# Performance work log

Measured on AMD Instinct MI355X. Metric: run time of the kernel, lower is better.

Reference implementation:

```python
import jax, jax.numpy as jnp
import numpy as np

D_IN = 1024
D_OUT = 1024
NUM_HEADS = 16
HEAD_DIM = D_OUT // NUM_HEADS


def setup_inputs() -> dict:
    key = jax.random.key(0)
    ks = jax.random.split(key, 6)
    B, S = 2, 2048
    scale = 1.0 / np.sqrt(D_IN)
    x = jax.random.normal(ks[0], (B, S, D_IN), dtype=jnp.float32)
    # Linear weights stored torch-style as [out_features, in_features]
    Wq = jax.random.normal(ks[1], (D_OUT, D_IN), dtype=jnp.float32) * scale
    Wk = jax.random.normal(ks[2], (D_OUT, D_IN), dtype=jnp.float32) * scale
    Wv = jax.random.normal(ks[3], (D_OUT, D_IN), dtype=jnp.float32) * scale
    Wo = jax.random.normal(ks[4], (D_OUT, D_IN), dtype=jnp.float32) * scale
    bo = jax.random.normal(ks[5], (D_OUT,), dtype=jnp.float32) * 0.01
    return {"x": x, "Wq": Wq, "Wk": Wk, "Wv": Wv, "Wo": Wo, "bo": bo}


def reference(x, Wq, Wk, Wv, Wo, bo):
    B, S, _ = x.shape
    H, hd = NUM_HEADS, HEAD_DIM
    # QKV projections (qkv_bias=False), split into heads: [B, H, S, hd]
    q = (x @ Wq.T).reshape(B, S, H, hd).transpose(0, 2, 1, 3)
    k = (x @ Wk.T).reshape(B, S, H, hd).transpose(0, 2, 1, 3)
    v = (x @ Wv.T).reshape(B, S, H, hd).transpose(0, 2, 1, 3)
    # scaled causal attention scores [B, H, S, S]
    scores = jnp.einsum("bhqd,bhkd->bhqk", q, k) / jnp.sqrt(jnp.float32(hd))
    causal = jnp.tril(jnp.ones((S, S), dtype=bool))
    scores = jnp.where(causal, scores, jnp.finfo(scores.dtype).min)
    attn = jax.nn.softmax(scores, axis=-1)  # dropout p=0.0 -> identity
    ctx = jnp.einsum("bhqk,bhkd->bhqd", attn, v)  # [B, H, S, hd]
    ctx = ctx.transpose(0, 2, 1, 3).reshape(B, S, H * hd)
    return ctx @ Wo.T + bo
```

## Files before the change

kernel.cpp:

```cpp
#include <hip/hip_runtime.h>
#include <hip/hip_bf16.h>

#define AS1 __attribute__((address_space(1)))
#define AS3 __attribute__((address_space(3)))

typedef __attribute__((ext_vector_type(4))) float floatx4;
typedef __attribute__((ext_vector_type(8))) short bf16x8;
typedef unsigned short u16;
typedef unsigned int u32;

__device__ __forceinline__ u16 f2b(float f) {
  u32 u = __builtin_bit_cast(u32, f);
  u += 0x7fffu + ((u >> 16) & 1u);
  return (u16)(u >> 16);
}
__device__ __forceinline__ u32 pk2(float lo, float hi) {
  __hip_bfloat162 h = __float22bfloat162_rn(float2{lo, hi});
  u32 u;
  __builtin_memcpy(&u, &h, 4);
  return u;
}
__device__ __forceinline__ bf16x8 cvt8(float4 a, float4 b) {
  uint4 u{pk2(a.x, a.y), pk2(a.z, a.w), pk2(b.x, b.y), pk2(b.z, b.w)};
  return __builtin_bit_cast(bf16x8, u);
}

__device__ __forceinline__ void gld16(const void* g, AS3 u32* l) {
  __builtin_amdgcn_global_load_lds((const AS1 u32*)(const AS1 void*)g, l, 16,
                                   0, 0);
}

#define QSCALE 0.18033688011112042f
#define QSHIFT 14.4269504088896f

__global__ __launch_bounds__(256) void cvt_all(
    const float* __restrict__ x, const float* __restrict__ wq,
    const float* __restrict__ wk, const float* __restrict__ wv,
    const float* __restrict__ wo, u16* __restrict__ xb, u16* __restrict__ wqb,
    u16* __restrict__ wkb, u16* __restrict__ wvb, u16* __restrict__ wob) {
  const int i = blockIdx.x * 256 + threadIdx.x;
  const float* src;
  u16* dst;
  int off;
  if (i < 524288) {
    src = x; dst = xb; off = i;
  } else {
    const int j = i - 524288;
    const int wsel = j >> 17;
    off = j & 131071;
    src = (wsel == 0) ? wq : (wsel == 1) ? wk : (wsel == 2) ? wv : wo;
    dst = (wsel == 0) ? wqb : (wsel == 1) ? wkb : (wsel == 2) ? wvb : wob;
  }
  const float4* p = (const float4*)(src + (size_t)off * 8);
  *(bf16x8*)(dst + (size_t)off * 8) = cvt8(p[0], p[1]);
}

__device__ __forceinline__ void gemm_bf16(const u16* __restrict__ A,
                                          const u16* __restrict__ B, short* sA,
                                          short* sB, floatx4 acc[4][4]) {
  const int tid = threadIdx.x;
  const int lane = tid & 63;
  const int w = tid >> 6;
  const int l15 = lane & 15, quad = lane >> 4;
  const int wm = w >> 1, wn = w & 1;

  const u16* ga = A + ((size_t)(w * 32 + (lane >> 2))) * 1024 + (lane & 3) * 8;
  const u16* gb = B + ((size_t)(w * 32 + (lane >> 2))) * 1024 + (lane & 3) * 8;
  AS3 u32* la = (AS3 u32*)(AS3 short*)sA + w * 512;
  AS3 u32* lb = (AS3 u32*)(AS3 short*)sB + w * 512;

  for (int kt = 0; kt < 32; ++kt) {
    __syncthreads();
    gld16(ga, la);
    gld16(ga + (size_t)16 * 1024, la + 256);
    gld16(gb, lb);
    gld16(gb + (size_t)16 * 1024, lb + 256);
    ga += 32;
    gb += 32;
    __syncthreads();

    bf16x8 af[4], bfr[4];
#pragma unroll
    for (int mc = 0; mc < 4; ++mc)
      af[mc] = *(const bf16x8*)&sA[(wm * 64 + mc * 16 + l15) * 32 + quad * 8];
#pragma unroll
    for (int nc = 0; nc < 4; ++nc)
      bfr[nc] = *(const bf16x8*)&sB[(wn * 64 + nc * 16 + l15) * 32 + quad * 8];
#pragma unroll
    for (int mc = 0; mc < 4; ++mc)
#pragma unroll
      for (int nc = 0; nc < 4; ++nc)
        acc[mc][nc] = __builtin_amdgcn_mfma_f32_16x16x32_bf16(
            af[mc], bfr[nc], acc[mc][nc], 0, 0, 0);
  }
}

__device__ __forceinline__ void qkv_epilogue(floatx4 acc[4][4], int m0, int nb,
                                             int sel, u16* __restrict__ Q,
                                             u16* __restrict__ K,
                                             u16* __restrict__ Vt) {
  const int tid = threadIdx.x;
  const int lane = tid & 63, w = tid >> 6;
  const int l15 = lane & 15, quad = lane >> 4;
  const int wm = w >> 1, wn = w & 1;
#pragma unroll
  for (int mc = 0; mc < 4; ++mc) {
#pragma unroll
    for (int nc = 0; nc < 4; ++nc) {
      const int nn = nb + wn * 64 + nc * 16 + l15;
      const int h = nn >> 6, d = nn & 63;
#pragma unroll
      for (int r = 0; r < 4; ++r) {
        const int m = m0 + wm * 64 + mc * 16 + quad * 4 + r;
        const int b = m >> 11, s = m & 2047;
        const int bh = b * 16 + h;
        float av = acc[mc][nc][r];
        if (sel == 0) av *= QSCALE;
        const u16 v = f2b(av);
        if (sel == 0)
          Q[((size_t)bh * 2048 + s) * 64 + d] = v;
        else if (sel == 1)
          K[((size_t)bh * 2048 + s) * 64 + d] = v;
        else
          Vt[((size_t)bh * 64 + d) * 2048 + s] = v;
      }
    }
  }
}

__global__ __launch_bounds__(256) void qkv_gemm_b(
    const u16* __restrict__ xb, const u16* __restrict__ Wqb,
    const u16* __restrict__ Wkb, const u16* __restrict__ Wvb,
    u16* __restrict__ Q, u16* __restrict__ K, u16* __restrict__ Vt) {
  __shared__ __align__(16) short smem[2 * 128 * 32];
  const int m0 = blockIdx.x * 128;
  const int by = blockIdx.y;
  const int sel = by >> 3;
  const int nb = (by & 7) * 128;
  const u16* W = (sel == 0) ? Wqb : (sel == 1) ? Wkb : Wvb;

  floatx4 acc[4][4];
#pragma unroll
  for (int i = 0; i < 4; i++)
#pragma unroll
    for (int j = 0; j < 4; j++) acc[i][j] = (floatx4)0.0f;
  gemm_bf16(xb + (size_t)m0 * 1024, W + (size_t)nb * 1024, smem,
            smem + 128 * 32, acc);
  qkv_epilogue(acc, m0, nb, sel, Q, K, Vt);
}

__global__ __launch_bounds__(256) void out_gemm_b(const u16* __restrict__ ctx,
                                                  const u16* __restrict__ Wob,
                                                  const float* __restrict__ bo,
                                                  float* __restrict__ out) {
  __shared__ __align__(16) short smem[128 * 32 + 64 * 32];
  const int tid = threadIdx.x;
  const int lane = tid & 63, w = tid >> 6;
  const int l15 = lane & 15, quad = lane >> 4;
  const int m0 = blockIdx.x * 128;
  const int n0 = blockIdx.y * 64;
  short* sA = smem;
  short* sB = smem + 128 * 32;

  const u16* ga = ctx + ((size_t)(m0 + w * 32 + (lane >> 2))) * 1024 +
                  (lane & 3) * 8;
  const u16* gb = Wob + ((size_t)(n0 + w * 16 + (lane >> 2))) * 1024 +
                  (lane & 3) * 8;
  AS3 u32* la = (AS3 u32*)(AS3 short*)sA + w * 512;
  AS3 u32* lb = (AS3 u32*)(AS3 short*)sB + w * 256;

  floatx4 acc[2][4];
#pragma unroll
  for (int i = 0; i < 2; i++)
#pragma unroll
    for (int j = 0; j < 4; j++) acc[i][j] = (floatx4)0.0f;

  for (int kt = 0; kt < 32; ++kt) {
    __syncthreads();
    gld16(ga, la);
    gld16(ga + (size_t)16 * 1024, la + 256);
    gld16(gb, lb);
    ga += 32;
    gb += 32;
    __syncthreads();

    bf16x8 af[2], bfr[4];
#pragma unroll
    for (int mc = 0; mc < 2; ++mc)
      af[mc] = *(const bf16x8*)&sA[(w * 32 + mc * 16 + l15) * 32 + quad * 8];
#pragma unroll
    for (int nc = 0; nc < 4; ++nc)
      bfr[nc] = *(const bf16x8*)&sB[(nc * 16 + l15) * 32 + quad * 8];
#pragma unroll
    for (int mc = 0; mc < 2; ++mc)
#pragma unroll
      for (int nc = 0; nc < 4; ++nc)
        acc[mc][nc] = __builtin_amdgcn_mfma_f32_16x16x32_bf16(
            af[mc], bfr[nc], acc[mc][nc], 0, 0, 0);
  }

#pragma unroll
  for (int mc = 0; mc < 2; ++mc)
#pragma unroll
    for (int nc = 0; nc < 4; ++nc) {
      const int n = n0 + nc * 16 + l15;
      const float bias = bo[n];
#pragma unroll
      for (int r = 0; r < 4; ++r) {
        const int m = m0 + w * 32 + mc * 16 + quad * 4 + r;
        out[(size_t)m * 1024 + n] = acc[mc][nc][r] + bias;
      }
    }
}

template <bool F32A>
__device__ __forceinline__ void gemm128(const void* __restrict__ A,
                                        const float* __restrict__ B, short* sA,
                                        short* sB, floatx4 acc[4][4]) {
  const int tid = threadIdx.x;
  const int lane = tid & 63;
  const int w = tid >> 6;
  const int l15 = lane & 15, quad = lane >> 4;
  const int wm = w >> 1, wn = w & 1;
  const int srow = tid >> 1;
  const int scb = (tid & 1) * 16;

  float4 pa[4], pb[4];
  int4 pa16[2];
  if constexpr (F32A) {
    const float* ap = (const float*)A + (size_t)srow * 1024 + scb;
    pa[0] = ((const float4*)ap)[0]; pa[1] = ((const float4*)ap)[1];
    pa[2] = ((const float4*)ap)[2]; pa[3] = ((const float4*)ap)[3];
  } else {
    const u16* ap = (const u16*)A + (size_t)srow * 1024 + scb;
    pa16[0] = ((const int4*)ap)[0]; pa16[1] = ((const int4*)ap)[1];
  }
  {
    const float* bp = B + (size_t)srow * 1024 + scb;
    pb[0] = ((const float4*)bp)[0]; pb[1] = ((const float4*)bp)[1];
    pb[2] = ((const float4*)bp)[2]; pb[3] = ((const float4*)bp)[3];
  }

  for (int kt = 0; kt < 32; ++kt) {
    __syncthreads();
    if constexpr (F32A) {
      *(bf16x8*)&sA[srow * 40 + scb] = cvt8(pa[0], pa[1]);
      *(bf16x8*)&sA[srow * 40 + scb + 8] = cvt8(pa[2], pa[3]);
    } else {
      *(int4*)&sA[srow * 40 + scb] = pa16[0];
      *(int4*)&sA[srow * 40 + scb + 8] = pa16[1];
    }
    *(bf16x8*)&sB[srow * 40 + scb] = cvt8(pb[0], pb[1]);
    *(bf16x8*)&sB[srow * 40 + scb + 8] = cvt8(pb[2], pb[3]);
    __syncthreads();

    if (kt < 31) {
      const int k0 = (kt + 1) * 32;
      if constexpr (F32A) {
        const float* ap = (const float*)A + (size_t)srow * 1024 + k0 + scb;
        pa[0] = ((const float4*)ap)[0]; pa[1] = ((const float4*)ap)[1];
        pa[2] = ((const float4*)ap)[2]; pa[3] = ((const float4*)ap)[3];
      } else {
        const u16* ap = (const u16*)A + (size_t)srow * 1024 + k0 + scb;
        pa16[0] = ((const int4*)ap)[0]; pa16[1] = ((const int4*)ap)[1];
      }
      const float* bp = B + (size_t)srow * 1024 + k0 + scb;
      pb[0] = ((const float4*)bp)[0]; pb[1] = ((const float4*)bp)[1];
      pb[2] = ((const float4*)bp)[2]; pb[3] = ((const float4*)bp)[3];
    }

    bf16x8 af[4], bfr[4];
#pragma unroll
    for (int mc = 0; mc < 4; ++mc)
      af[mc] = *(const bf16x8*)&sA[(wm * 64 + mc * 16 + l15) * 40 + quad * 8];
#pragma unroll
    for (int nc = 0; nc < 4; ++nc)
      bfr[nc] = *(const bf16x8*)&sB[(wn * 64 + nc * 16 + l15) * 40 + quad * 8];
#pragma unroll
    for (int mc = 0; mc < 4; ++mc)
#pragma unroll
      for (int nc = 0; nc < 4; ++nc)
        acc[mc][nc] = __builtin_amdgcn_mfma_f32_16x16x32_bf16(
            af[mc], bfr[nc], acc[mc][nc], 0, 0, 0);
  }
}

__global__ __launch_bounds__(256) void qkv_gemm_f(
    const float* __restrict__ x, const float* __restrict__ Wq,
    const float* __restrict__ Wk, const float* __restrict__ Wv,
    u16* __restrict__ Q, u16* __restrict__ K, u16* __restrict__ Vt) {
  __shared__ __align__(16) short smem[2 * 128 * 40];
  const int m0 = blockIdx.x * 128;
  const int by = blockIdx.y;
  const int sel = by >> 3;
  const int nb = (by & 7) * 128;
  const float* W = (sel == 0) ? Wq : (sel == 1) ? Wk : Wv;

  floatx4 acc[4][4];
#pragma unroll
  for (int i = 0; i < 4; i++)
#pragma unroll
    for (int j = 0; j < 4; j++) acc[i][j] = (floatx4)0.0f;
  gemm128<true>((const void*)(x + (size_t)m0 * 1024), W + (size_t)nb * 1024,
                smem, smem + 128 * 40, acc);
  qkv_epilogue(acc, m0, nb, sel, Q, K, Vt);
}

__global__ __launch_bounds__(256) void out_gemm_f(const u16* __restrict__ ctx,
                                                  const float* __restrict__ Wo,
                                                  const float* __restrict__ bo,
                                                  float* __restrict__ out) {
  __shared__ __align__(16) short smem[2 * 128 * 40];
  const int tid = threadIdx.x;
  const int lane = tid & 63, w = tid >> 6;
  const int l15 = lane & 15, quad = lane >> 4;
  const int wm = w >> 1, wn = w & 1;
  const int m0 = blockIdx.x * 128;
  const int n0 = blockIdx.y * 128;

  floatx4 acc[4][4];
#pragma unroll
  for (int i = 0; i < 4; i++)
#pragma unroll
    for (int j = 0; j < 4; j++) acc[i][j] = (floatx4)0.0f;
  gemm128<false>((const void*)(ctx + (size_t)m0 * 1024),
                 Wo + (size_t)n0 * 1024, smem, smem + 128 * 40, acc);

#pragma unroll
  for (int mc = 0; mc < 4; ++mc)
#pragma unroll
    for (int nc = 0; nc < 4; ++nc) {
      const int n = n0 + wn * 64 + nc * 16 + l15;
      const float bias = bo[n];
#pragma unroll
      for (int r = 0; r < 4; ++r) {
        const int m = m0 + wm * 64 + mc * 16 + quad * 4 + r;
        out[(size_t)m * 1024 + n] = acc[mc][nc][r] + bias;
      }
    }
}

__global__ __launch_bounds__(512, 2) void attn_kernel(
    const u16* __restrict__ Q, const u16* __restrict__ K,
    const u16* __restrict__ Vt, u16* __restrict__ ctx) {
  const int bid = blockIdx.x;
  const int pr = bid >> 5;
  const int bh = bid & 31;
  const int tid = threadIdx.x;
  const int w = tid >> 6;
  const int lane = tid & 63;
  const int l15 = lane & 15;
  const int quad = lane >> 4;

  constexpr int KE = 128 * 72;
  constexpr int VE = 64 * 136;
  constexpr int BUF = KE + VE;
  __shared__ __align__(16) u16 lds[2 * BUF];

  const int kr = tid >> 2, kc = (tid & 3) * 16;
  const int vd = tid >> 3, vc = (tid & 7) * 16;
  const int b = bh >> 4, h = bh & 15;

  const u16* Kg = K + (size_t)bh * 2048 * 64;
  const u16* Vg = Vt + (size_t)bh * 64 * 2048;

  int4 pk[2], pv[2];
  pk[0] = *(const int4*)(Kg + (size_t)kr * 64 + kc);
  pk[1] = *(const int4*)(Kg + (size_t)kr * 64 + kc + 8);
  pv[0] = *(const int4*)(Vg + (size_t)vd * 2048 + vc);
  pv[1] = *(const int4*)(Vg + (size_t)vd * 2048 + vc + 8);
  *(int4*)&lds[kr * 72 + kc] = pk[0];
  *(int4*)&lds[kr * 72 + kc + 8] = pk[1];
  *(int4*)&lds[KE + vd * 136 + vc] = pv[0];
  *(int4*)&lds[KE + vd * 136 + vc + 8] = pv[1];
  __syncthreads();
  int cur = 0;

  for (int half = 0; half < 2; ++half) {
    const int c = half ? pr : (15 - pr);
    const int wrow = c * 128 + w * 16;

    bf16x8 aQ0, aQ1;
    {
      const u16* qp = Q + ((size_t)bh * 2048 + wrow + l15) * 64 + quad * 8;
      aQ0 = *(const bf16x8*)(qp);
      aQ1 = *(const bf16x8*)(qp + 32);
    }

    floatx4 accOT[4];
#pragma unroll
    for (int i = 0; i < 4; ++i) accOT[i] = (floatx4)0.0f;
    floatx4 lsv = (floatx4)0.0f;

    for (int jb = 0; jb <= c; ++jb) {
      const u16* sKb = lds + cur * BUF;
      const u16* sVb = sKb + KE;

      const int jn = (jb < c) ? (jb + 1) * 128 : (half == 0 ? 0 : -1);
      if (jn >= 0) {
        pk[0] = *(const int4*)(Kg + (size_t)(jn + kr) * 64 + kc);
        pk[1] = *(const int4*)(Kg + (size_t)(jn + kr) * 64 + kc + 8);
        pv[0] = *(const int4*)(Vg + (size_t)vd * 2048 + jn + vc);
        pv[1] = *(const int4*)(Vg + (size_t)vd * 2048 + jn + vc + 8);
      }

      if (jb < c) {
        bf16x8 ka[2][4];
        uint2 va[2][8];
#pragma unroll
        for (int u = 0; u < 4; ++u) {
          const u16* kp0 = sKb + (0 * 32 + l15) * 72 + quad * 8;
          ka[0][u] = *(const bf16x8*)(kp0 + (u >> 1) * (16 * 72) + (u & 1) * 32);
        }
#pragma unroll
        for (int dt = 0; dt < 4; ++dt) {
          const u16* vp = sVb + (dt * 16 + l15) * 136 + 0 * 32 + quad * 4;
          va[0][2 * dt] = *(const uint2*)(vp);
          va[0][2 * dt + 1] = *(const uint2*)(vp + 16);
        }
#pragma unroll
        for (int kp = 0; kp < 4; ++kp) {
          const int pc = kp & 1, pn = (kp + 1) & 1;
          if (kp < 3) {
            const u16* kp1 = sKb + ((kp + 1) * 32 + l15) * 72 + quad * 8;
#pragma unroll
            for (int u = 0; u < 4; ++u)
              ka[pn][u] =
                  *(const bf16x8*)(kp1 + (u >> 1) * (16 * 72) + (u & 1) * 32);
#pragma unroll
            for (int dt = 0; dt < 4; ++dt) {
              const u16* vp =
                  sVb + (dt * 16 + l15) * 136 + (kp + 1) * 32 + quad * 4;
              va[pn][2 * dt] = *(const uint2*)(vp);
              va[pn][2 * dt + 1] = *(const uint2*)(vp + 16);
            }
          }
          floatx4 st0 = (floatx4)0.0f, st1 = (floatx4)0.0f;
          __builtin_amdgcn_s_setprio(1);
          st0 = __builtin_amdgcn_mfma_f32_16x16x32_bf16(ka[pc][0], aQ0, st0,
                                                        0, 0, 0);
          st1 = __builtin_amdgcn_mfma_f32_16x16x32_bf16(ka[pc][2], aQ0, st1,
                                                        0, 0, 0);
          st0 = __builtin_amdgcn_mfma_f32_16x16x32_bf16(ka[pc][1], aQ1, st0,
                                                        0, 0, 0);
          st1 = __builtin_amdgcn_mfma_f32_16x16x32_bf16(ka[pc][3], aQ1, st1,
                                                        0, 0, 0);
          __builtin_amdgcn_s_setprio(0);
          float p0[4], p1[4];
#pragma unroll
          for (int r = 0; r < 4; ++r) {
            p0[r] = __builtin_amdgcn_exp2f(st0[r] - QSHIFT);
            p1[r] = __builtin_amdgcn_exp2f(st1[r] - QSHIFT);
          }
#pragma unroll
          for (int r = 0; r < 4; ++r) lsv[r] += p0[r] + p1[r];
          uint4 pfu{pk2(p0[0], p0[1]), pk2(p0[2], p0[3]), pk2(p1[0], p1[1]),
                    pk2(p1[2], p1[3])};
          const bf16x8 pf8 = __builtin_bit_cast(bf16x8, pfu);
          __builtin_amdgcn_s_setprio(1);
#pragma unroll
          for (int dt = 0; dt < 4; ++dt) {
            uint4 avu{va[pc][2 * dt].x, va[pc][2 * dt].y, va[pc][2 * dt + 1].x,
                      va[pc][2 * dt + 1].y};
            bf16x8 av8 = __builtin_bit_cast(bf16x8, avu);
            accOT[dt] = __builtin_amdgcn_mfma_f32_16x16x32_bf16(
                av8, pf8, accOT[dt], 0, 0, 0);
          }
          __builtin_amdgcn_s_setprio(0);
        }
      } else {
        const int jbase = c * 128;
#pragma unroll 2
        for (int kp = 0; kp < 4; ++kp) {
          const int kbase = jbase + kp * 32;
          if (kbase > wrow + 15) break;

          const u16* kr0 = sKb + (kp * 32 + l15) * 72 + quad * 8;
          bf16x8 ak00 = *(const bf16x8*)(kr0);
          bf16x8 ak01 = *(const bf16x8*)(kr0 + 32);
          floatx4 st0 = (floatx4)0.0f;
          st0 = __builtin_amdgcn_mfma_f32_16x16x32_bf16(ak00, aQ0, st0, 0, 0,
                                                        0);
          st0 = __builtin_amdgcn_mfma_f32_16x16x32_bf16(ak01, aQ1, st0, 0, 0,
                                                        0);

          const bool have1 = (kbase + 16 <= wrow + 15);
          floatx4 st1 = (floatx4)0.0f;
          if (have1) {
            const u16* kr1 = kr0 + 16 * 72;
            bf16x8 ak10 = *(const bf16x8*)(kr1);
            bf16x8 ak11 = *(const bf16x8*)(kr1 + 32);
            st1 = __builtin_amdgcn_mfma_f32_16x16x32_bf16(ak10, aQ0, st1, 0,
                                                          0, 0);
            st1 = __builtin_amdgcn_mfma_f32_16x16x32_bf16(ak11, aQ1, st1, 0,
                                                          0, 0);
          }

          float p0[4], p1[4];
          const bool m0b = (kbase + 15 > wrow);
#pragma unroll
          for (int r = 0; r < 4; ++r) {
            float t = st0[r] - QSHIFT;
            if (m0b && (kbase + quad * 4 + r > wrow + l15)) t = -1e30f;
            p0[r] = __builtin_amdgcn_exp2f(t);
          }
          if (have1) {
            const bool m1b = (kbase + 31 > wrow);
#pragma unroll
            for (int r = 0; r < 4; ++r) {
              float t = st1[r] - QSHIFT;
              if (m1b && (kbase + 16 + quad * 4 + r > wrow + l15)) t = -1e30f;
              p1[r] = __builtin_amdgcn_exp2f(t);
            }
          } else {
            p1[0] = p1[1] = p1[2] = p1[3] = 0.0f;
          }
#pragma unroll
          for (int r = 0; r < 4; ++r) lsv[r] += p0[r] + p1[r];

          uint4 pfu{pk2(p0[0], p0[1]), pk2(p0[2], p0[3]), pk2(p1[0], p1[1]),
                    pk2(p1[2], p1[3])};
          const bf16x8 pf8 = __builtin_bit_cast(bf16x8, pfu);

#pragma unroll
          for (int dt = 0; dt < 4; ++dt) {
            const u16* vp = sVb + (dt * 16 + l15) * 136 + kp * 32 + quad * 4;
            uint2 v0 = *(const uint2*)(vp);
            uint2 v1 = *(const uint2*)(vp + 16);
            uint4 avu{v0.x, v0.y, v1.x, v1.y};
            bf16x8 av8 = __builtin_bit_cast(bf16x8, avu);
            accOT[dt] = __builtin_amdgcn_mfma_f32_16x16x32_bf16(
                av8, pf8, accOT[dt], 0, 0, 0);
          }
        }
      }

      if (jn >= 0) {
        u16* dK = lds + (cur ^ 1) * BUF;
        u16* dV = dK + KE;
        *(int4*)&dK[kr * 72 + kc] = pk[0];
        *(int4*)&dK[kr * 72 + kc + 8] = pk[1];
        *(int4*)&dV[vd * 136 + vc] = pv[0];
        *(int4*)&dV[vd * 136 + vc + 8] = pv[1];
      }
      __syncthreads();
      cur ^= 1;
    }

    float lsum = (lsv[0] + lsv[1]) + (lsv[2] + lsv[3]);
    lsum += __shfl_xor(lsum, 16, 64);
    lsum += __shfl_xor(lsum, 32, 64);

    const float inv = 1.0f / lsum;
    u16* tw = lds + (cur ^ 1) * BUF + (w * 16) * 72;
#pragma unroll
    for (int dt = 0; dt < 4; ++dt) {
      uint2 o2{pk2(accOT[dt][0] * inv, accOT[dt][1] * inv),
               pk2(accOT[dt][2] * inv, accOT[dt][3] * inv)};
      *(uint2*)&tw[l15 * 72 + dt * 16 + quad * 4] = o2;
    }
    bf16x8 o0 = *(const bf16x8*)&tw[l15 * 72 + quad * 16];
    bf16x8 o1 = *(const bf16x8*)&tw[l15 * 72 + quad * 16 + 8];
    u16* cp = ctx + ((size_t)(b * 2048 + wrow + l15)) * 1024 + h * 64 +
              quad * 16;
    *(bf16x8*)cp = o0;
    *(bf16x8*)(cp + 8) = o1;
    __syncthreads();
  }
}

extern "C" void kernel_launch(void* const* d_in, const int* in_sizes, int n_in,
                              void* d_out, int out_size, void* d_ws,
                              size_t ws_size, hipStream_t stream) {
  const float* x = (const float*)d_in[0];
  const float* Wq = (const float*)d_in[1];
  const float* Wk = (const float*)d_in[2];
  const float* Wv = (const float*)d_in[3];
  const float* Wo = (const float*)d_in[4];
  const float* bo = (const float*)d_in[5];
  float* out = (float*)d_out;

  u16* Q = (u16*)d_ws;
  u16* K = Q + (size_t)4096 * 1024;
  u16* Vt = K + (size_t)4096 * 1024;
  u16* ctx = Vt + (size_t)4096 * 1024;

  if (ws_size >= (size_t)40 * 1024 * 1024) {
    u16* xb = ctx;
    u16* Wqb = (u16*)d_ws + (size_t)16 * 1024 * 1024;
    u16* Wkb = Wqb + (size_t)1024 * 1024;
    u16* Wvb = Wkb + (size_t)1024 * 1024;
    u16* Wob = Wvb + (size_t)1024 * 1024;

    cvt_all<<<4096, 256, 0, stream>>>(x, Wq, Wk, Wv, Wo, xb, Wqb, Wkb, Wvb,
                                      Wob);
    qkv_gemm_b<<<dim3(32, 24), 256, 0, stream>>>(xb, Wqb, Wkb, Wvb, Q, K, Vt);
    attn_kernel<<<256, 512, 0, stream>>>(Q, K, Vt, ctx);
    out_gemm_b<<<dim3(32, 16), 256, 0, stream>>>(ctx, Wob, bo, out);
  } else {
    qkv_gemm_f<<<dim3(32, 24), 256, 0, stream>>>(x, Wq, Wk, Wv, Q, K, Vt);
    attn_kernel<<<256, 512, 0, stream>>>(Q, K, Vt, ctx);
    out_gemm_f<<<dim3(32, 8), 256, 0, stream>>>(ctx, Wo, bo, out);
  }
}
```

Baseline: 196.3 us.

## Process both paired causal query chunks in one pass over K/V tiles

```diff
diff --git a/kernel.cpp b/kernel.cpp
--- a/kernel.cpp
+++ b/kernel.cpp
@@ -340,6 +340,163 @@
     }
 }
 
+template <bool CLEAN>
+__device__ __forceinline__ void attn_tile(const u16* __restrict__ sKb,
+                                          const u16* __restrict__ sVb,
+                                          const int l15, const int quad,
+                                          const int jbase, const int wrow,
+                                          const bf16x8 aQ0, const bf16x8 aQ1,
+                                          floatx4 (&acc)[4], floatx4& lsv) {
+  if constexpr (CLEAN) {
+    bf16x8 ka[2][4];
+    uint2 va[2][8];
+#pragma unroll
+    for (int u = 0; u < 4; ++u) {
+      const u16* kp0 = sKb + l15 * 72 + quad * 8;
+      ka[0][u] = *(const bf16x8*)(kp0 + (u >> 1) * (16 * 72) + (u & 1) * 32);
+    }
+#pragma unroll
+    for (int dt = 0; dt < 4; ++dt) {
+      const u16* vp = sVb + (dt * 16 + l15) * 136 + quad * 4;
+      va[0][2 * dt] = *(const uint2*)(vp);
+      va[0][2 * dt + 1] = *(const uint2*)(vp + 16);
+    }
+#pragma unroll
+    for (int kp = 0; kp < 4; ++kp) {
+      const int pc = kp & 1, pn = (kp + 1) & 1;
+      if (kp < 3) {
+        const u16* kp1 = sKb + ((kp + 1) * 32 + l15) * 72 + quad * 8;
+#pragma unroll
+        for (int u = 0; u < 4; ++u)
+          ka[pn][u] =
+              *(const bf16x8*)(kp1 + (u >> 1) * (16 * 72) + (u & 1) * 32);
+#pragma unroll
+        for (int dt = 0; dt < 4; ++dt) {
+          const u16* vp =
+              sVb + (dt * 16 + l15) * 136 + (kp + 1) * 32 + quad * 4;
+          va[pn][2 * dt] = *(const uint2*)(vp);
+          va[pn][2 * dt + 1] = *(const uint2*)(vp + 16);
+        }
+      }
+      floatx4 st0 = (floatx4)0.0f, st1 = (floatx4)0.0f;
+      __builtin_amdgcn_s_setprio(1);
+      st0 = __builtin_amdgcn_mfma_f32_16x16x32_bf16(ka[pc][0], aQ0, st0, 0, 0,
+                                                    0);
+      st1 = __builtin_amdgcn_mfma_f32_16x16x32_bf16(ka[pc][2], aQ0, st1, 0, 0,
+                                                    0);
+      st0 = __builtin_amdgcn_mfma_f32_16x16x32_bf16(ka[pc][1], aQ1, st0, 0, 0,
+                                                    0);
+      st1 = __builtin_amdgcn_mfma_f32_16x16x32_bf16(ka[pc][3], aQ1, st1, 0, 0,
+                                                    0);
+      __builtin_amdgcn_s_setprio(0);
+      float p0[4], p1[4];
+#pragma unroll
+      for (int r = 0; r < 4; ++r) {
+        p0[r] = __builtin_amdgcn_exp2f(st0[r] - QSHIFT);
+        p1[r] = __builtin_amdgcn_exp2f(st1[r] - QSHIFT);
+      }
+#pragma unroll
+      for (int r = 0; r < 4; ++r) lsv[r] += p0[r] + p1[r];
+      uint4 pfu{pk2(p0[0], p0[1]), pk2(p0[2], p0[3]), pk2(p1[0], p1[1]),
+                pk2(p1[2], p1[3])};
+      const bf16x8 pf8 = __builtin_bit_cast(bf16x8, pfu);
+      __builtin_amdgcn_s_setprio(1);
+#pragma unroll
+      for (int dt = 0; dt < 4; ++dt) {
+        uint4 avu{va[pc][2 * dt].x, va[pc][2 * dt].y, va[pc][2 * dt + 1].x,
+                  va[pc][2 * dt + 1].y};
+        bf16x8 av8 = __builtin_bit_cast(bf16x8, avu);
+        acc[dt] = __builtin_amdgcn_mfma_f32_16x16x32_bf16(av8, pf8, acc[dt],
+                                                          0, 0, 0);
+      }
+      __builtin_amdgcn_s_setprio(0);
+    }
+  } else {
+#pragma unroll 2
+    for (int kp = 0; kp < 4; ++kp) {
+      const int kbase = jbase + kp * 32;
+      if (kbase > wrow + 15) break;
+
+      const u16* kr0 = sKb + (kp * 32 + l15) * 72 + quad * 8;
+      bf16x8 ak00 = *(const bf16x8*)(kr0);
+      bf16x8 ak01 = *(const bf16x8*)(kr0 + 32);
+      floatx4 st0 = (floatx4)0.0f;
+      st0 = __builtin_amdgcn_mfma_f32_16x16x32_bf16(ak00, aQ0, st0, 0, 0, 0);
+      st0 = __builtin_amdgcn_mfma_f32_16x16x32_bf16(ak01, aQ1, st0, 0, 0, 0);
+
+      const bool have1 = (kbase + 16 <= wrow + 15);
+      floatx4 st1 = (floatx4)0.0f;
+      if (have1) {
+        const u16* kr1 = kr0 + 16 * 72;
+        bf16x8 ak10 = *(const bf16x8*)(kr1);
+        bf16x8 ak11 = *(const bf16x8*)(kr1 + 32);
+        st1 = __builtin_amdgcn_mfma_f32_16x16x32_bf16(ak10, aQ0, st1, 0, 0, 0);
+        st1 = __builtin_amdgcn_mfma_f32_16x16x32_bf16(ak11, aQ1, st1, 0, 0, 0);
+      }
+
+      float p0[4], p1[4];
+      const bool m0b = (kbase + 15 > wrow);
+#pragma unroll
+      for (int r = 0; r < 4; ++r) {
+        float t = st0[r] - QSHIFT;
+        if (m0b && (kbase + quad * 4 + r > wrow + l15)) t = -1e30f;
+        p0[r] = __builtin_amdgcn_exp2f(t);
+      }
+      if (have1) {
+        const bool m1b = (kbase + 31 > wrow);
+#pragma unroll
+        for (int r = 0; r < 4; ++r) {
+          float t = st1[r] - QSHIFT;
+          if (m1b && (kbase + 16 + quad * 4 + r > wrow + l15)) t = -1e30f;
+          p1[r] = __builtin_amdgcn_exp2f(t);
+        }
+      } else {
+        p1[0] = p1[1] = p1[2] = p1[3] = 0.0f;
+      }
+#pragma unroll
+      for (int r = 0; r < 4; ++r) lsv[r] += p0[r] + p1[r];
+
+      uint4 pfu{pk2(p0[0], p0[1]), pk2(p0[2], p0[3]), pk2(p1[0], p1[1]),
+                pk2(p1[2], p1[3])};
+      const bf16x8 pf8 = __builtin_bit_cast(bf16x8, pfu);
+
+#pragma unroll
+      for (int dt = 0; dt < 4; ++dt) {
+        const u16* vp = sVb + (dt * 16 + l15) * 136 + kp * 32 + quad * 4;
+        uint2 v0 = *(const uint2*)(vp);
+        uint2 v1 = *(const uint2*)(vp + 16);
+        uint4 avu{v0.x, v0.y, v1.x, v1.y};
+        bf16x8 av8 = __builtin_bit_cast(bf16x8, avu);
+        acc[dt] = __builtin_amdgcn_mfma_f32_16x16x32_bf16(av8, pf8, acc[dt],
+                                                          0, 0, 0);
+      }
+    }
+  }
+}
+
+__device__ __forceinline__ void attn_write(u16* tw, const floatx4 (&acc)[4],
+                                           const floatx4 lsv, const int l15,
+                                           const int quad, const int wrow,
+                                           const int b, const int h,
+                                           u16* __restrict__ ctx) {
+  float lsum = (lsv[0] + lsv[1]) + (lsv[2] + lsv[3]);
+  lsum += __shfl_xor(lsum, 16, 64);
+  lsum += __shfl_xor(lsum, 32, 64);
+  const float inv = 1.0f / lsum;
+#pragma unroll
+  for (int dt = 0; dt < 4; ++dt) {
+    uint2 o2{pk2(acc[dt][0] * inv, acc[dt][1] * inv),
+             pk2(acc[dt][2] * inv, acc[dt][3] * inv)};
+    *(uint2*)&tw[l15 * 72 + dt * 16 + quad * 4] = o2;
+  }
+  bf16x8 o0 = *(const bf16x8*)&tw[l15 * 72 + quad * 16];
+  bf16x8 o1 = *(const bf16x8*)&tw[l15 * 72 + quad * 16 + 8];
+  u16* cp =
+      ctx + ((size_t)(b * 2048 + wrow + l15)) * 1024 + h * 64 + quad * 16;
+  *(bf16x8*)cp = o0;
+  *(bf16x8*)(cp + 8) = o1;
+}
+
 __global__ __launch_bounds__(512, 2) void attn_kernel(
     const u16* __restrict__ Q, const u16* __restrict__ K,
     const u16* __restrict__ Vt, u16* __restrict__ ctx) {
@@ -364,6 +521,28 @@
   const u16* Kg = K + (size_t)bh * 2048 * 64;
   const u16* Vg = Vt + (size_t)bh * 64 * 2048;
 
+  const int cA = 15 - pr, cB = pr;
+  const int wrowA = cA * 128 + w * 16;
+  const int wrowB = cB * 128 + w * 16;
+
+  bf16x8 aQA0, aQA1, aQB0, aQB1;
+  {
+    const u16* qa = Q + ((size_t)bh * 2048 + wrowA + l15) * 64 + quad * 8;
+    aQA0 = *(const bf16x8*)(qa);
+    aQA1 = *(const bf16x8*)(qa + 32);
+    const u16* qb = Q + ((size_t)bh * 2048 + wrowB + l15) * 64 + quad * 8;
+    aQB0 = *(const bf16x8*)(qb);
+    aQB1 = *(const bf16x8*)(qb + 32);
+  }
+
+  floatx4 accA[4], accB[4];
+#pragma unroll
+  for (int i = 0; i < 4; ++i) {
+    accA[i] = (floatx4)0.0f;
+    accB[i] = (floatx4)0.0f;
+  }
+  floatx4 lsvA = (floatx4)0.0f, lsvB = (floatx4)0.0f;
+
   int4 pk[2], pv[2];
   pk[0] = *(const int4*)(Kg + (size_t)kr * 64 + kc);
   pk[1] = *(const int4*)(Kg + (size_t)kr * 64 + kc + 8);
@@ -376,197 +555,47 @@
   __syncthreads();
   int cur = 0;
 
-  for (int half = 0; half < 2; ++half) {
-    const int c = half ? pr : (15 - pr);
-    const int wrow = c * 128 + w * 16;
-
-    bf16x8 aQ0, aQ1;
-    {
-      const u16* qp = Q + ((size_t)bh * 2048 + wrow + l15) * 64 + quad * 8;
-      aQ0 = *(const bf16x8*)(qp);
-      aQ1 = *(const bf16x8*)(qp + 32);
-    }
-
-    floatx4 accOT[4];
-#pragma unroll
-    for (int i = 0; i < 4; ++i) accOT[i] = (floatx4)0.0f;
-    floatx4 lsv = (floatx4)0.0f;
-
-    for (int jb = 0; jb <= c; ++jb) {
-      const u16* sKb = lds + cur * BUF;
-      const u16* sVb = sKb + KE;
-
-      const int jn = (jb < c) ? (jb + 1) * 128 : (half == 0 ? 0 : -1);
-      if (jn >= 0) {
-        pk[0] = *(const int4*)(Kg + (size_t)(jn + kr) * 64 + kc);
-        pk[1] = *(const int4*)(Kg + (size_t)(jn + kr) * 64 + kc + 8);
-        pv[0] = *(const int4*)(Vg + (size_t)vd * 2048 + jn + vc);
-        pv[1] = *(const int4*)(Vg + (size_t)vd * 2048 + jn + vc + 8);
-      }
-
-      if (jb < c) {
-        bf16x8 ka[2][4];
-        uint2 va[2][8];
-#pragma unroll
-        for (int u = 0; u < 4; ++u) {
-          const u16* kp0 = sKb + (0 * 32 + l15) * 72 + quad * 8;
-          ka[0][u] = *(const bf16x8*)(kp0 + (u >> 1) * (16 * 72) + (u & 1) * 32);
-        }
-#pragma unroll
-        for (int dt = 0; dt < 4; ++dt) {
-          const u16* vp = sVb + (dt * 16 + l15) * 136 + 0 * 32 + quad * 4;
-          va[0][2 * dt] = *(const uint2*)(vp);
-          va[0][2 * dt + 1] = *(const uint2*)(vp + 16);
-        }
-#pragma unroll
-        for (int kp = 0; kp < 4; ++kp) {
-          const int pc = kp & 1, pn = (kp + 1) & 1;
-          if (kp < 3) {
-            const u16* kp1 = sKb + ((kp + 1) * 32 + l15) * 72 + quad * 8;
-#pragma unroll
-            for (int u = 0; u < 4; ++u)
-              ka[pn][u] =
-                  *(const bf16x8*)(kp1 + (u >> 1) * (16 * 72) + (u & 1) * 32);
-#pragma unroll
-            for (int dt = 0; dt < 4; ++dt) {
-              const u16* vp =
-                  sVb + (dt * 16 + l15) * 136 + (kp + 1) * 32 + quad * 4;
-              va[pn][2 * dt] = *(const uint2*)(vp);
-              va[pn][2 * dt + 1] = *(const uint2*)(vp + 16);
-            }
-          }
-          floatx4 st0 = (floatx4)0.0f, st1 = (floatx4)0.0f;
-          __builtin_amdgcn_s_setprio(1);
-          st0 = __builtin_amdgcn_mfma_f32_16x16x32_bf16(ka[pc][0], aQ0, st0,
-                                                        0, 0, 0);
-          st1 = __builtin_amdgcn_mfma_f32_16x16x32_bf16(ka[pc][2], aQ0, st1,
-                                                        0, 0, 0);
-          st0 = __builtin_amdgcn_mfma_f32_16x16x32_bf16(ka[pc][1], aQ1, st0,
-                                                        0, 0, 0);
-          st1 = __builtin_amdgcn_mfma_f32_16x16x32_bf16(ka[pc][3], aQ1, st1,
-                                                        0, 0, 0);
-          __builtin_amdgcn_s_setprio(0);
-          float p0[4], p1[4];
-#pragma unroll
-          for (int r = 0; r < 4; ++r) {
-            p0[r] = __builtin_amdgcn_exp2f(st0[r] - QSHIFT);
-            p1[r] = __builtin_amdgcn_exp2f(st1[r] - QSHIFT);
-          }
-#pragma unroll
-          for (int r = 0; r < 4; ++r) lsv[r] += p0[r] + p1[r];
-          uint4 pfu{pk2(p0[0], p0[1]), pk2(p0[2], p0[3]), pk2(p1[0], p1[1]),
-                    pk2(p1[2], p1[3])};
-          const bf16x8 pf8 = __builtin_bit_cast(bf16x8, pfu);
-          __builtin_amdgcn_s_setprio(1);
-#pragma unroll
-          for (int dt = 0; dt < 4; ++dt) {
-            uint4 avu{va[pc][2 * dt].x, va[pc][2 * dt].y, va[pc][2 * dt + 1].x,
-                      va[pc][2 * dt + 1].y};
-            bf16x8 av8 = __builtin_bit_cast(bf16x8, avu);
-            accOT[dt] = __builtin_amdgcn_mfma_f32_16x16x32_bf16(
-                av8, pf8, accOT[dt], 0, 0, 0);
-          }
-          __builtin_amdgcn_s_setprio(0);
-        }
-      } else {
-        const int jbase = c * 128;
-#pragma unroll 2
-        for (int kp = 0; kp < 4; ++kp) {
-          const int kbase = jbase + kp * 32;
-          if (kbase > wrow + 15) break;
-
-          const u16* kr0 = sKb + (kp * 32 + l15) * 72 + quad * 8;
-          bf16x8 ak00 = *(const bf16x8*)(kr0);
-          bf16x8 ak01 = *(const bf16x8*)(kr0 + 32);
-          floatx4 st0 = (floatx4)0.0f;
-          st0 = __builtin_amdgcn_mfma_f32_16x16x32_bf16(ak00, aQ0, st0, 0, 0,
-                                                        0);
-          st0 = __builtin_amdgcn_mfma_f32_16x16x32_bf16(ak01, aQ1, st0, 0, 0,
-                                                        0);
-
-          const bool have1 = (kbase + 16 <= wrow + 15);
-          floatx4 st1 = (floatx4)0.0f;
-          if (have1) {
-            const u16* kr1 = kr0 + 16 * 72;
-            bf16x8 ak10 = *(const bf16x8*)(kr1);
-            bf16x8 ak11 = *(const bf16x8*)(kr1 + 32);
-            st1 = __builtin_amdgcn_mfma_f32_16x16x32_bf16(ak10, aQ0, st1, 0,
-                                                          0, 0);
-            st1 = __builtin_amdgcn_mfma_f32_16x16x32_bf16(ak11, aQ1, st1, 0,
-                                                          0, 0);
-          }
-
-          float p0[4], p1[4];
-          const bool m0b = (kbase + 15 > wrow);
-#pragma unroll
-          for (int r = 0; r < 4; ++r) {
-            float t = st0[r] - QSHIFT;
-            if (m0b && (kbase + quad * 4 + r > wrow + l15)) t = -1e30f;
-            p0[r] = __builtin_amdgcn_exp2f(t);
-          }
-          if (have1) {
-            const bool m1b = (kbase + 31 > wrow);
-#pragma unroll
-            for (int r = 0; r < 4; ++r) {
-              float t = st1[r] - QSHIFT;
-              if (m1b && (kbase + 16 + quad * 4 + r > wrow + l15)) t = -1e30f;
-              p1[r] = __builtin_amdgcn_exp2f(t);
-            }
-          } else {
-            p1[0] = p1[1] = p1[2] = p1[3] = 0.0f;
-          }
-#pragma unroll
-          for (int r = 0; r < 4; ++r) lsv[r] += p0[r] + p1[r];
-
-          uint4 pfu{pk2(p0[0], p0[1]), pk2(p0[2], p0[3]), pk2(p1[0], p1[1]),
-                    pk2(p1[2], p1[3])};
-          const bf16x8 pf8 = __builtin_bit_cast(bf16x8, pfu);
-
-#pragma unroll
-          for (int dt = 0; dt < 4; ++dt) {
-            const u16* vp = sVb + (dt * 16 + l15) * 136 + kp * 32 + quad * 4;
-            uint2 v0 = *(const uint2*)(vp);
-            uint2 v1 = *(const uint2*)(vp + 16);
-            uint4 avu{v0.x, v0.y, v1.x, v1.y};
-            bf16x8 av8 = __builtin_bit_cast(bf16x8, avu);
-            accOT[dt] = __builtin_amdgcn_mfma_f32_16x16x32_bf16(
-                av8, pf8, accOT[dt], 0, 0, 0);
-          }
-        }
-      }
-
-      if (jn >= 0) {
-        u16* dK = lds + (cur ^ 1) * BUF;
-        u16* dV = dK + KE;
-        *(int4*)&dK[kr * 72 + kc] = pk[0];
-        *(int4*)&dK[kr * 72 + kc + 8] = pk[1];
-        *(int4*)&dV[vd * 136 + vc] = pv[0];
-        *(int4*)&dV[vd * 136 + vc + 8] = pv[1];
-      }
-      __syncthreads();
-      cur ^= 1;
-    }
-
-    float lsum = (lsv[0] + lsv[1]) + (lsv[2] + lsv[3]);
-    lsum += __shfl_xor(lsum, 16, 64);
-    lsum += __shfl_xor(lsum, 32, 64);
-
-    const float inv = 1.0f / lsum;
-    u16* tw = lds + (cur ^ 1) * BUF + (w * 16) * 72;
-#pragma unroll
-    for (int dt = 0; dt < 4; ++dt) {
-      uint2 o2{pk2(accOT[dt][0] * inv, accOT[dt][1] * inv),
-               pk2(accOT[dt][2] * inv, accOT[dt][3] * inv)};
-      *(uint2*)&tw[l15 * 72 + dt * 16 + quad * 4] = o2;
-    }
-    bf16x8 o0 = *(const bf16x8*)&tw[l15 * 72 + quad * 16];
-    bf16x8 o1 = *(const bf16x8*)&tw[l15 * 72 + quad * 16 + 8];
-    u16* cp = ctx + ((size_t)(b * 2048 + wrow + l15)) * 1024 + h * 64 +
-              quad * 16;
-    *(bf16x8*)cp = o0;
-    *(bf16x8*)(cp + 8) = o1;
+  for (int jb = 0; jb <= cA; ++jb) {
+    const u16* sKb = lds + cur * BUF;
+    const u16* sVb = sKb + KE;
+
+    const int jn = (jb < cA) ? (jb + 1) * 128 : -1;
+    if (jn >= 0) {
+      pk[0] = *(const int4*)(Kg + (size_t)(jn + kr) * 64 + kc);
+      pk[1] = *(const int4*)(Kg + (size_t)(jn + kr) * 64 + kc + 8);
+      pv[0] = *(const int4*)(Vg + (size_t)vd * 2048 + jn + vc);
+      pv[1] = *(const int4*)(Vg + (size_t)vd * 2048 + jn + vc + 8);
+    }
+
+    const int jbase = jb * 128;
+    if (jb < cA)
+      attn_tile<true>(sKb, sVb, l15, quad, jbase, wrowA, aQA0, aQA1, accA,
+                      lsvA);
+    else
+      attn_tile<false>(sKb, sVb, l15, quad, jbase, wrowA, aQA0, aQA1, accA,
+                       lsvA);
+    if (jb < cB)
+      attn_tile<true>(sKb, sVb, l15, quad, jbase, wrowB, aQB0, aQB1, accB,
+                      lsvB);
+    else if (jb == cB)
+      attn_tile<false>(sKb, sVb, l15, quad, jbase, wrowB, aQB0, aQB1, accB,
+                       lsvB);
+
+    if (jn >= 0) {
+      u16* dK = lds + (cur ^ 1) * BUF;
+      u16* dV = dK + KE;
+      *(int4*)&dK[kr * 72 + kc] = pk[0];
+      *(int4*)&dK[kr * 72 + kc + 8] = pk[1];
+      *(int4*)&dV[vd * 136 + vc] = pv[0];
+      *(int4*)&dV[vd * 136 + vc + 8] = pv[1];
+    }
     __syncthreads();
-  }
+    cur ^= 1;
+  }
+
+  u16* tw = lds + (cur ^ 1) * BUF + (w * 16) * 72;
+  attn_write(tw, accA, lsvA, l15, quad, wrowA, b, h, ctx);
+  attn_write(tw, accB, lsvB, l15, quad, wrowB, b, h, ctx);
 }
 
 extern "C" void kernel_launch(void* const* d_in, const int* in_sizes, int n_in,
```

Result: no change. 194.9 us (-0.7%).
